# Performance work log

Measured on AMD Instinct MI355X. Metric: run time of the kernel, lower is better.

Reference implementation:

```python
import jax, jax.numpy as jnp
import numpy as np

N, C = 65536, 100
TEMP = 2.0


def setup_inputs() -> dict:
    key = jax.random.key(0)
    ks = jax.random.split(key, 7)
    inp = {}
    names = ["outputs1", "outputs2", "outputs3", "outputs4", "outputs5", "mimic"]
    for k, name in zip(ks[:6], names):
        inp[name] = jax.random.normal(k, (N, C), dtype=jnp.float32)
    inp["targets"] = jax.random.randint(ks[6], (N,), 0, C, dtype=jnp.int64)
    inp["n_test"] = N
    return inp


def _margin(x, targets):
    # top-2 values per row; margin = top1-top2 if the target class is the argmax, else 0
    top2, _ = jax.lax.top_k(x, 2)  # [N, 2]
    tgt_val = jnp.take_along_axis(x, targets[:, None], axis=1)[:, 0]  # [N]
    return jnp.where(tgt_val == top2[:, 0], top2[:, 0] - top2[:, 1],
                     jnp.zeros((), dtype=x.dtype))


def reference(outputs1, outputs2, outputs3, outputs4, outputs5, mimic, targets, n_test):
    margins = jnp.stack(
        [_margin(o, targets) for o in (outputs1, outputs2, outputs3, outputs4, outputs5, mimic)],
        axis=-1,
    )  # [n_test, 6]
    out_threshold = jax.nn.softmax(margins / TEMP, axis=-1)
    max_preds = jnp.max(jnp.stack([outputs1, outputs2, outputs3, outputs4, outputs5], axis=0))
    return (max_preds, out_threshold)
```

## Files before the change

kernel.cpp:

```cpp
#include <hip/hip_runtime.h>


constexpr int C = 100;
constexpr float INV_TEMP = 0.5f;

__device__ __forceinline__ unsigned enc_f(float f) {
    unsigned u = __float_as_uint(f);
    return (u & 0x80000000u) ? ~u : (u | 0x80000000u);
}

__global__ __launch_bounds__(256) void margin_kernel(
    const float* __restrict__ o1, const float* __restrict__ o2,
    const float* __restrict__ o3, const float* __restrict__ o4,
    const float* __restrict__ o5, const float* __restrict__ mimic,
    const int* __restrict__ tgt, float* __restrict__ out,
    unsigned* __restrict__ ws, int n)
{
    __shared__ unsigned wmax[4];

    const int m    = blockIdx.y;
    const int tid2 = blockIdx.x * 256 + threadIdx.x;
    const int row  = tid2 >> 1;
    const int half = tid2 & 1;
    const int lane = threadIdx.x & 63;

    const float* __restrict__ mat =
        (m == 0) ? o1 : (m == 1) ? o2 : (m == 2) ? o3 :
        (m == 3) ? o4 : (m == 4) ? o5 : mimic;

    const int pidx  = 2 * lane + 1;
    const int probe = (pidx < n) ? tgt[pidx] : 0;
    const unsigned long long nz = __ballot(probe != 0);
    const int tstride = (nz == 0ull) ? 2 : 1;

    float rowM1 = -INFINITY;

    if (row < n) {
        const size_t rowoff = (size_t)row * C;
        const float4* __restrict__ p4 =
            (const float4*)(mat + rowoff) + (half ? 13 : 0);

        float m1x = -INFINITY, m2x = -INFINITY;
        float m1y = -INFINITY, m2y = -INFINITY;
        float m1z = -INFINITY, m2z = -INFINITY;
        float m1w = -INFINITY, m2w = -INFINITY;
        #pragma unroll
        for (int i = 0; i < 12; ++i) {
            const float4 v = p4[i];
            m2x = fmaxf(m2x, fminf(m1x, v.x)); m1x = fmaxf(m1x, v.x);
            m2y = fmaxf(m2y, fminf(m1y, v.y)); m1y = fmaxf(m1y, v.y);
            m2z = fmaxf(m2z, fminf(m1z, v.z)); m1z = fmaxf(m1z, v.z);
            m2w = fmaxf(m2w, fminf(m1w, v.w)); m1w = fmaxf(m1w, v.w);
        }
        if (!half) {
            const float4 v = p4[12];
            m2x = fmaxf(m2x, fminf(m1x, v.x)); m1x = fmaxf(m1x, v.x);
            m2y = fmaxf(m2y, fminf(m1y, v.y)); m1y = fmaxf(m1y, v.y);
            m2z = fmaxf(m2z, fminf(m1z, v.z)); m1z = fmaxf(m1z, v.z);
            m2w = fmaxf(m2w, fminf(m1w, v.w)); m1w = fmaxf(m1w, v.w);
        }
        const float m1xy = fmaxf(m1x, m1y);
        const float m2xy = fmaxf(fminf(m1x, m1y), fmaxf(m2x, m2y));
        const float m1zw = fmaxf(m1z, m1w);
        const float m2zw = fmaxf(fminf(m1z, m1w), fmaxf(m2z, m2w));
        const float tm1  = fmaxf(m1xy, m1zw);
        const float tm2  = fmaxf(fminf(m1xy, m1zw), fmaxf(m2xy, m2zw));

        const float p1 = __shfl_xor(tm1, 1);
        const float p2 = __shfl_xor(tm2, 1);
        const float M1 = fmaxf(tm1, p1);
        const float M2 = fmaxf(fminf(tm1, p1), fmaxf(tm2, p2));

        const int   t  = tgt[(size_t)row * tstride];
        const float tv = mat[rowoff + t];
        if (!half)
            out[1 + (size_t)row * 6 + m] = (tv == M1) ? (M1 - M2) * INV_TEMP : 0.0f;
        rowM1 = M1;
    }

    #pragma unroll
    for (int s = 1; s < 64; s <<= 1) rowM1 = fmaxf(rowM1, __shfl_xor(rowM1, s));
    if (m < 5) {
        if (lane == 0) wmax[threadIdx.x >> 6] = enc_f(rowM1);
        __syncthreads();
        if (threadIdx.x == 0) {
            const unsigned u = max(max(wmax[0], wmax[1]), max(wmax[2], wmax[3]));
            atomicMax(ws, u);
        }
    }
}

__global__ __launch_bounds__(256) void softmax_kernel(
    float* __restrict__ out, const unsigned* __restrict__ ws, int n)
{
    const int row = blockIdx.x * blockDim.x + threadIdx.x;
    if (row < n) {
        float* p = out + 1 + (size_t)row * 6;
        float mrg[6];
        #pragma unroll
        for (int j = 0; j < 6; ++j) mrg[j] = p[j];
        float mx = mrg[0];
        #pragma unroll
        for (int j = 1; j < 6; ++j) mx = fmaxf(mx, mrg[j]);
        float e[6], s = 0.0f;
        #pragma unroll
        for (int j = 0; j < 6; ++j) { e[j] = __expf(mrg[j] - mx); s += e[j]; }
        const float inv = 1.0f / s;
        #pragma unroll
        for (int j = 0; j < 6; ++j) p[j] = e[j] * inv;
    }
    if (row == 0) {
        const unsigned e = ws[0];
        const unsigned bits = (e & 0x80000000u) ? (e & 0x7FFFFFFFu) : ~e;
        out[0] = __uint_as_float(bits);
    }
}

extern "C" void kernel_launch(void* const* d_in, const int* in_sizes, int n_in,
                              void* d_out, int out_size, void* d_ws, size_t ws_size,
                              hipStream_t stream) {
    const float* o1    = (const float*)d_in[0];
    const float* o2    = (const float*)d_in[1];
    const float* o3    = (const float*)d_in[2];
    const float* o4    = (const float*)d_in[3];
    const float* o5    = (const float*)d_in[4];
    const float* mimic = (const float*)d_in[5];
    const int*   tgt   = (const int*)d_in[6];
    float*       out   = (float*)d_out;
    unsigned*    ws    = (unsigned*)d_ws;

    const int n = in_sizes[6];

    hipMemsetAsync(ws, 0, sizeof(unsigned), stream);

    dim3 grid((2 * n + 255) / 256, 6);
    margin_kernel<<<grid, 256, 0, stream>>>(o1, o2, o3, o4, o5, mimic,
                                            tgt, out, ws, n);
    softmax_kernel<<<(n + 255) / 256, 256, 0, stream>>>(out, ws, n);
}
```

Before: 186.4 us.

## Stage row tiles into LDS with async global-to-LDS copies for coalesced loads

Each block now copies a contiguous 64-row tile of the matrix into shared memory using global_load_lds 16-byte async copies, then four threads per row compute the top-2 values from LDS and combine them with shuffles. The target value is also read from LDS instead of by a second global gather. This replaces strided per-thread float4 global reads with fully coalesced bulk transfers. The cost is 25.6 KB of LDS per block, which limits occupancy, plus a barrier before any compute can start.

```diff
diff --git a/kernel.cpp b/kernel.cpp
--- a/kernel.cpp
+++ b/kernel.cpp
@@ -1,12 +1,20 @@
 #include <hip/hip_runtime.h>
 
 
-constexpr int C = 100;
+constexpr int C       = 100;
+constexpr int ROWS    = 64;
 constexpr float INV_TEMP = 0.5f;
 
 __device__ __forceinline__ unsigned enc_f(float f) {
     unsigned u = __float_as_uint(f);
     return (u & 0x80000000u) ? ~u : (u | 0x80000000u);
+}
+
+__device__ __forceinline__ void async_cp16(const float* g, float* l) {
+    __builtin_amdgcn_global_load_lds(
+        (const __attribute__((address_space(1))) void*)g,
+        (__attribute__((address_space(3))) void*)l,
+        16, 0, 0);
 }
 
 __global__ __launch_bounds__(256) void margin_kernel(
@@ -16,13 +24,12 @@
     const int* __restrict__ tgt, float* __restrict__ out,
     unsigned* __restrict__ ws, int n)
 {
+    __shared__ float    tile[ROWS * C];
     __shared__ unsigned wmax[4];
 
     const int m    = blockIdx.y;
-    const int tid2 = blockIdx.x * 256 + threadIdx.x;
-    const int row  = tid2 >> 1;
-    const int half = tid2 & 1;
-    const int lane = threadIdx.x & 63;
+    const int tid  = threadIdx.x;
+    const int lane = tid & 63;
 
     const float* __restrict__ mat =
         (m == 0) ? o1 : (m == 1) ? o2 : (m == 2) ? o3 :
@@ -33,60 +40,60 @@
     const unsigned long long nz = __ballot(probe != 0);
     const int tstride = (nz == 0ull) ? 2 : 1;
 
-    float rowM1 = -INFINITY;
+    const size_t base   = (size_t)blockIdx.x * (ROWS * C);
+    const size_t maxIdx = (size_t)n * C - 4;
+    #pragma unroll
+    for (int c = 0; c < 6; ++c) {
+        const int    off = (c * 256 + tid) * 4;
+        const size_t g   = base + (size_t)off;
+        async_cp16(mat + (g <= maxIdx ? g : maxIdx), tile + off);
+    }
+    if (tid < 64) {
+        const int    off = 6 * 1024 + tid * 4;
+        const size_t g   = base + (size_t)off;
+        async_cp16(mat + (g <= maxIdx ? g : maxIdx), tile + off);
+    }
+    __syncthreads();
 
-    if (row < n) {
-        const size_t rowoff = (size_t)row * C;
-        const float4* __restrict__ p4 =
-            (const float4*)(mat + rowoff) + (half ? 13 : 0);
+    const int rl  = tid >> 2;
+    const int q   = tid & 3;
+    const int row = blockIdx.x * ROWS + rl;
 
-        float m1x = -INFINITY, m2x = -INFINITY;
-        float m1y = -INFINITY, m2y = -INFINITY;
-        float m1z = -INFINITY, m2z = -INFINITY;
-        float m1w = -INFINITY, m2w = -INFINITY;
-        #pragma unroll
-        for (int i = 0; i < 12; ++i) {
-            const float4 v = p4[i];
-            m2x = fmaxf(m2x, fminf(m1x, v.x)); m1x = fmaxf(m1x, v.x);
-            m2y = fmaxf(m2y, fminf(m1y, v.y)); m1y = fmaxf(m1y, v.y);
-            m2z = fmaxf(m2z, fminf(m1z, v.z)); m1z = fmaxf(m1z, v.z);
-            m2w = fmaxf(m2w, fminf(m1w, v.w)); m1w = fmaxf(m1w, v.w);
-        }
-        if (!half) {
-            const float4 v = p4[12];
-            m2x = fmaxf(m2x, fminf(m1x, v.x)); m1x = fmaxf(m1x, v.x);
-            m2y = fmaxf(m2y, fminf(m1y, v.y)); m1y = fmaxf(m1y, v.y);
-            m2z = fmaxf(m2z, fminf(m1z, v.z)); m1z = fmaxf(m1z, v.z);
-            m2w = fmaxf(m2w, fminf(m1w, v.w)); m1w = fmaxf(m1w, v.w);
-        }
-        const float m1xy = fmaxf(m1x, m1y);
-        const float m2xy = fmaxf(fminf(m1x, m1y), fmaxf(m2x, m2y));
-        const float m1zw = fmaxf(m1z, m1w);
-        const float m2zw = fmaxf(fminf(m1z, m1w), fmaxf(m2z, m2w));
-        const float tm1  = fmaxf(m1xy, m1zw);
-        const float tm2  = fmaxf(fminf(m1xy, m1zw), fmaxf(m2xy, m2zw));
+    const float* p = tile + rl * C + q * 25;
+    float a1 = -INFINITY, a2 = -INFINITY;
+    float b1 = -INFINITY, b2 = -INFINITY;
+    #pragma unroll
+    for (int i = 0; i < 12; ++i) {
+        const float va = p[2 * i], vb = p[2 * i + 1];
+        a2 = fmaxf(a2, fminf(a1, va)); a1 = fmaxf(a1, va);
+        b2 = fmaxf(b2, fminf(b1, vb)); b1 = fmaxf(b1, vb);
+    }
+    { const float v = p[24]; a2 = fmaxf(a2, fminf(a1, v)); a1 = fmaxf(a1, v); }
+    float m1 = fmaxf(a1, b1);
+    float m2 = fmaxf(fminf(a1, b1), fmaxf(a2, b2));
 
-        const float p1 = __shfl_xor(tm1, 1);
-        const float p2 = __shfl_xor(tm2, 1);
-        const float M1 = fmaxf(tm1, p1);
-        const float M2 = fmaxf(fminf(tm1, p1), fmaxf(tm2, p2));
-
-        const int   t  = tgt[(size_t)row * tstride];
-        const float tv = mat[rowoff + t];
-        if (!half)
-            out[1 + (size_t)row * 6 + m] = (tv == M1) ? (M1 - M2) * INV_TEMP : 0.0f;
-        rowM1 = M1;
+    #pragma unroll
+    for (int s = 1; s <= 2; s <<= 1) {
+        const float p1 = __shfl_xor(m1, s);
+        const float p2 = __shfl_xor(m2, s);
+        m2 = fmaxf(fminf(m1, p1), fmaxf(m2, p2));
+        m1 = fmaxf(m1, p1);
     }
 
+    if (q == 0 && row < n) {
+        const int   t  = tgt[(size_t)row * tstride];
+        const float tv = tile[rl * C + t];
+        out[1 + (size_t)row * 6 + m] = (tv == m1) ? (m1 - m2) * INV_TEMP : 0.0f;
+    }
+
+    float gm = (row < n) ? m1 : -INFINITY;
     #pragma unroll
-    for (int s = 1; s < 64; s <<= 1) rowM1 = fmaxf(rowM1, __shfl_xor(rowM1, s));
+    for (int s = 1; s < 64; s <<= 1) gm = fmaxf(gm, __shfl_xor(gm, s));
     if (m < 5) {
-        if (lane == 0) wmax[threadIdx.x >> 6] = enc_f(rowM1);
+        if (lane == 0) wmax[tid >> 6] = enc_f(gm);
         __syncthreads();
-        if (threadIdx.x == 0) {
-            const unsigned u = max(max(wmax[0], wmax[1]), max(wmax[2], wmax[3]));
-            atomicMax(ws, u);
-        }
+        if (tid == 0)
+            atomicMax(ws, max(max(wmax[0], wmax[1]), max(wmax[2], wmax[3])));
     }
 }
 
@@ -133,7 +140,7 @@
 
     hipMemsetAsync(ws, 0, sizeof(unsigned), stream);
 
-    dim3 grid((2 * n + 255) / 256, 6);
+    dim3 grid((n + ROWS - 1) / ROWS, 6);
     margin_kernel<<<grid, 256, 0, stream>>>(o1, o2, o3, o4, o5, mimic,
                                             tgt, out, ws, n);
     softmax_kernel<<<(n + 255) / 256, 256, 0, stream>>>(out, ws, n);
```

After: 205.8 us. 1.1x slower.
